# Kernel optimization log

Hardware: AMD Instinct MI355X
Metric: run time of the kernel (lower is better)

The kernel has to match this reference:

```python
import jax, jax.numpy as jnp
import numpy as np

N = 8192      # number of nodes; input feature dim == N (identity-style features)
HID = 200     # hidden dim hard-coded in GCNConv(adj.shape[0], 200)
OUT = 5       # out_dim (sentiment classes)


def setup_inputs() -> dict:
    key = jax.random.key(0)
    k1, k2, k3, k4 = jax.random.split(key, 4)
    x = jax.random.normal(k1, (N, N), dtype=jnp.float32)
    adj = jax.random.uniform(k2, (N, N), dtype=jnp.float32)
    W1 = jax.random.normal(k3, (N, HID), dtype=jnp.float32) * (1.0 / np.sqrt(N))
    b1 = jnp.zeros((HID,), dtype=jnp.float32)
    W2 = jax.random.normal(k4, (HID, OUT), dtype=jnp.float32) * (1.0 / np.sqrt(HID))
    b2 = jnp.zeros((OUT,), dtype=jnp.float32)
    return {"x": x, "adj": adj, "W1": W1, "b1": b1, "W2": W2, "b2": b2}


def gcn_conv(adj, x, W, b):
    # support = X @ W (cheap, small output dim), then propagate: adj @ support
    return adj @ (x @ W) + b


def reference(x, adj, W1, b1, W2, b2):
    h = jax.nn.relu(gcn_conv(adj, x, W1, b1))      # [N, 200]
    logits = gcn_conv(adj, h, W2, b2)              # [N, 5]
    return jax.nn.softmax(logits, axis=-1)
```

## Files before the change

kernel.cpp:

```cpp
#include <hip/hip_runtime.h>
#include <hip/hip_fp16.h>
#include <math.h>

#define NN   8192
#define KD   8192
#define HID  200
#define NP   224
#define OUTC 5

#define BM   128
#define BK   32
#define KS   8
#define KCH  (KD / KS)
#define NT   (KCH / BK)
#define TUB  896

typedef _Float16 f16;
typedef __attribute__((ext_vector_type(4))) _Float16 f16x4;
typedef __attribute__((ext_vector_type(8))) _Float16 f16x8;
typedef __attribute__((ext_vector_type(4))) float f32x4;

__device__ __forceinline__ int swzu(int r, int c) {
    return (r * 4 + (c ^ (r & 3))) ^ (r & 4);
}

__device__ __forceinline__ void fill16(const f16* g, f16* l) {
    __builtin_amdgcn_global_load_lds(
        (const __attribute__((address_space(1))) void*)g,
        (__attribute__((address_space(3))) void*)l, 16, 0, 0);
}

__global__ __launch_bounds__(256) void k_prep_w1(const float* __restrict__ W1,
                                                 f16* __restrict__ Bsw) {
    __shared__ float tile[64][65];
    const int bx = blockIdx.x;
    const int n0 = blockIdx.y * 64;
    const int k0 = bx * 64;
    const int t = threadIdx.x;
    #pragma unroll
    for (int q = 0; q < 4; ++q) {
        int idx4 = t + q * 256;
        int kk = idx4 >> 4, nn4 = (idx4 & 15) * 4;
        int n = n0 + nn4;
        float4 v = {0.f, 0.f, 0.f, 0.f};
        if (n + 4 <= HID) v = *(const float4*)(W1 + (size_t)(k0 + kk) * HID + n);
        tile[kk][nn4 + 0] = v.x; tile[kk][nn4 + 1] = v.y;
        tile[kk][nn4 + 2] = v.z; tile[kk][nn4 + 3] = v.w;
    }
    __syncthreads();
    #pragma unroll
    for (int p2 = 0; p2 < 2; ++p2) {
        int u = t + p2 * 256;
        int rl = u >> 3, cc = u & 7;
        int ktl = cc >> 2, c = cc & 3;
        int r = n0 + rl;
        if (r < NP) {
            f16x8 o;
            #pragma unroll
            for (int h = 0; h < 8; ++h) o[h] = (f16)tile[ktl * 32 + c * 8 + h][rl];
            *(f16x8*)(Bsw + ((size_t)(bx * 2 + ktl) * TUB + swzu(r, c)) * 8) = o;
        }
    }
}

__global__ __launch_bounds__(512, 4) void k_gemm(const float* __restrict__ A,
                                                 const f16* __restrict__ Bsw,
                                                 f16* __restrict__ CP) {
    __shared__ __align__(16) f16 Af0[BM * BK], Af1[BM * BK];
    __shared__ __align__(16) f16 Bf0[NP * BK], Bf1[NP * BK];

    const int t = threadIdx.x;
    const int lane = t & 63, wv = t >> 6;
    const int wm = wv >> 1, wn = wv & 1;
    const int l15 = lane & 15, g = lane >> 4;
    const int bid = blockIdx.x;
    const int ky = bid & 7;
    const int bx = bid >> 3;
    const int m0 = bx * BM;
    const int kt0 = ky * NT;
    const size_t kc0 = (size_t)ky * KCH;

    const int ar = t >> 2, aq = t & 3;
    const int au = swzu(ar, aq) * 8;
    const float* ap = A + (size_t)(m0 + ar) * KD + kc0 + (size_t)aq * 8;
    const f16* bsrc = Bsw + ((size_t)kt0 * TUB + (size_t)(wv * 64 + lane)) * 8;

    const int a0o = swzu(wm * 32 + l15, g) * 8;
    const int bo0 = swzu(wn * 112 + l15, g) * 8;

    f32x4 acc[2][7];
    #pragma unroll
    for (int m = 0; m < 2; ++m)
        #pragma unroll
        for (int n = 0; n < 7; ++n) acc[m][n] = (f32x4){0.f, 0.f, 0.f, 0.f};

    float4 va0, va1, vb0, vb1;
#define LOADA(i, V0, V1) { const float* p_ = ap + (size_t)(i) * BK;  \
        V0 = *(const float4*)p_; V1 = *(const float4*)(p_ + 4); }
#define CONV_STORE(AF, V0, V1) { f16x8 hh_;                                   \
        hh_[0]=(f16)V0.x; hh_[1]=(f16)V0.y; hh_[2]=(f16)V0.z; hh_[3]=(f16)V0.w; \
        hh_[4]=(f16)V1.x; hh_[5]=(f16)V1.y; hh_[6]=(f16)V1.z; hh_[7]=(f16)V1.w; \
        *(f16x8*)&AF[au] = hh_; }
#define FILLB(i, BF) { const f16* bs_ = bsrc + (size_t)(i) * (TUB * 8);  \
        fill16(bs_, &BF[(wv * 64) * 8]);                                 \
        if (wv < 6) fill16(bs_ + 512 * 8, &BF[(512 + wv * 64) * 8]); }
#define MFMA_PH(AF, BF) {                                                \
        f16x8 a0_ = *(const f16x8*)&AF[a0o];                             \
        f16x8 a1_ = *(const f16x8*)&AF[a0o + 512];                       \
        _Pragma("unroll")                                                \
        for (int n = 0; n < 7; ++n) {                                    \
            f16x8 b_ = *(const f16x8*)&BF[bo0 + n * 512];                \
            acc[0][n] = __builtin_amdgcn_mfma_f32_16x16x32_f16(a0_, b_, acc[0][n], 0, 0, 0); \
            acc[1][n] = __builtin_amdgcn_mfma_f32_16x16x32_f16(a1_, b_, acc[1][n], 0, 0, 0); } }

    LOADA(0, va0, va1); LOADA(1, vb0, vb1);
    FILLB(0, Bf0);
    CONV_STORE(Af0, va0, va1);
    asm volatile("s_waitcnt vmcnt(0) lgkmcnt(0)\n\ts_barrier" ::: "memory");

    #pragma unroll 1
    for (int ip = 0; ip < NT / 2 - 1; ++ip) {
        const int i = 2 * ip;
        FILLB(i + 1, Bf1);
        CONV_STORE(Af1, vb0, vb1);
        LOADA(i + 2, va0, va1);
        __builtin_amdgcn_s_setprio(1);
        MFMA_PH(Af0, Bf0);
        __builtin_amdgcn_s_setprio(0);
        asm volatile("s_waitcnt vmcnt(2) lgkmcnt(0)\n\ts_barrier" ::: "memory");
        FILLB(i + 2, Bf0);
        CONV_STORE(Af0, va0, va1);
        LOADA(i + 3, vb0, vb1);
        __builtin_amdgcn_s_setprio(1);
        MFMA_PH(Af1, Bf1);
        __builtin_amdgcn_s_setprio(0);
        asm volatile("s_waitcnt vmcnt(2) lgkmcnt(0)\n\ts_barrier" ::: "memory");
    }
    FILLB(NT - 1, Bf1);
    CONV_STORE(Af1, vb0, vb1);
    __builtin_amdgcn_s_setprio(1);
    MFMA_PH(Af0, Bf0);
    __builtin_amdgcn_s_setprio(0);
    asm volatile("s_waitcnt vmcnt(0) lgkmcnt(0)\n\ts_barrier" ::: "memory");
    MFMA_PH(Af1, Bf1);
#undef LOADA
#undef CONV_STORE
#undef FILLB
#undef MFMA_PH

    f16* o = CP + (size_t)ky * ((size_t)NN * NP);
    #pragma unroll
    for (int m = 0; m < 2; ++m) {
        #pragma unroll
        for (int n = 0; n < 7; ++n) {
            int rb = m0 + wm * 32 + m * 16 + g * 4;
            int c = wn * 112 + n * 16 + l15;
            #pragma unroll
            for (int r = 0; r < 4; ++r)
                o[(size_t)(rb + r) * NP + c] = (f16)acc[m][n][r];
        }
    }
}

__global__ __launch_bounds__(256) void k_combine_b(const f16* __restrict__ CP,
                                                   f16* __restrict__ Bsw) {
    __shared__ float tile[64][65];
    const size_t SZ = (size_t)NN * NP;
    const int bx = blockIdx.x;
    const int n0 = blockIdx.y * 64;
    const int k0 = bx * 64;
    const int t = threadIdx.x;
    #pragma unroll
    for (int q = 0; q < 4; ++q) {
        int idx4 = t + q * 256;
        int kk = idx4 >> 4, nn4 = (idx4 & 15) * 4;
        int n = n0 + nn4;
        float s0 = 0.f, s1 = 0.f, s2 = 0.f, s3 = 0.f;
        if (n < NP) {
            #pragma unroll
            for (int p = 0; p < KS; ++p) {
                f16x4 v = *(const f16x4*)(CP + (size_t)p * SZ + (size_t)(k0 + kk) * NP + n);
                s0 += (float)v[0]; s1 += (float)v[1]; s2 += (float)v[2]; s3 += (float)v[3];
            }
        }
        tile[kk][nn4 + 0] = s0; tile[kk][nn4 + 1] = s1;
        tile[kk][nn4 + 2] = s2; tile[kk][nn4 + 3] = s3;
    }
    __syncthreads();
    #pragma unroll
    for (int p2 = 0; p2 < 2; ++p2) {
        int u = t + p2 * 256;
        int rl = u >> 3, cc = u & 7;
        int ktl = cc >> 2, c = cc & 3;
        int r = n0 + rl;
        if (r < NP) {
            f16x8 o;
            #pragma unroll
            for (int h = 0; h < 8; ++h) o[h] = (f16)tile[ktl * 32 + c * 8 + h][rl];
            *(f16x8*)(Bsw + ((size_t)(bx * 2 + ktl) * TUB + swzu(r, c)) * 8) = o;
        }
    }
}

__global__ __launch_bounds__(256) void k_tail(const f16* __restrict__ CP,
                                              const float* __restrict__ b1,
                                              const float* __restrict__ W2,
                                              float* __restrict__ S2T) {
    const int tx = threadIdx.x;
    const int ty = threadIdx.y;
    const int row = blockIdx.x * 8 + ty;
    float s[OUTC] = {0.f, 0.f, 0.f, 0.f, 0.f};
    if (tx < 28) {
        const size_t SZ = (size_t)NN * NP;
        const size_t off = (size_t)row * NP + tx * 8;
        float h[8] = {0.f,0.f,0.f,0.f,0.f,0.f,0.f,0.f};
        #pragma unroll
        for (int p = 0; p < KS; ++p) {
            f16x8 v = *(const f16x8*)(CP + (size_t)p * SZ + off);
            #pragma unroll
            for (int j = 0; j < 8; ++j) h[j] += (float)v[j];
        }
        #pragma unroll
        for (int j = 0; j < 8; ++j) {
            int c = tx * 8 + j;
            if (c < HID) {
                float hv = fmaxf(h[j] + b1[c], 0.f);
                #pragma unroll
                for (int q = 0; q < OUTC; ++q) s[q] += hv * W2[c * OUTC + q];
            }
        }
    }
    #pragma unroll
    for (int q = 0; q < OUTC; ++q)
        #pragma unroll
        for (int off2 = 16; off2; off2 >>= 1) s[q] += __shfl_down(s[q], off2, 32);
    if (tx == 0) {
        #pragma unroll
        for (int q = 0; q < OUTC; ++q) S2T[(size_t)q * NN + row] = s[q];
    }
}

__global__ __launch_bounds__(256) void k_final(const float* __restrict__ adj,
                                               const float* __restrict__ S2T,
                                               const float* __restrict__ b2,
                                               float* __restrict__ out) {
    __shared__ float red[4][8][OUTC];
    const int t = threadIdx.x, wave = t >> 6, lane = t & 63;
    const int row0 = blockIdx.x * 8;
    float acc[8][OUTC];
    #pragma unroll
    for (int r = 0; r < 8; ++r)
        #pragma unroll
        for (int c = 0; c < OUTC; ++c) acc[r][c] = 0.f;

    for (int jj = 0; jj < 8; ++jj) {
        int kb = (t + jj * 256) * 4;
        float4 s2[OUTC];
        #pragma unroll
        for (int c = 0; c < OUTC; ++c) s2[c] = *(const float4*)(S2T + (size_t)c * NN + kb);
        #pragma unroll
        for (int r = 0; r < 8; ++r) {
            float4 a = *(const float4*)(adj + (size_t)(row0 + r) * KD + kb);
            #pragma unroll
            for (int c = 0; c < OUTC; ++c)
                acc[r][c] += a.x * s2[c].x + a.y * s2[c].y + a.z * s2[c].z + a.w * s2[c].w;
        }
    }
    #pragma unroll
    for (int r = 0; r < 8; ++r)
        #pragma unroll
        for (int c = 0; c < OUTC; ++c) {
            float v = acc[r][c];
            #pragma unroll
            for (int off = 32; off; off >>= 1) v += __shfl_down(v, off, 64);
            if (lane == 0) red[wave][r][c] = v;
        }
    __syncthreads();
    if (t < 8) {
        int r = t;
        float lg[OUTC];
        #pragma unroll
        for (int c = 0; c < OUTC; ++c)
            lg[c] = red[0][r][c] + red[1][r][c] + red[2][r][c] + red[3][r][c] + b2[c];
        float mx = lg[0];
        #pragma unroll
        for (int c = 1; c < OUTC; ++c) mx = fmaxf(mx, lg[c]);
        float e[OUTC], ssum = 0.f;
        #pragma unroll
        for (int c = 0; c < OUTC; ++c) { e[c] = expf(lg[c] - mx); ssum += e[c]; }
        float inv = 1.0f / ssum;
        #pragma unroll
        for (int c = 0; c < OUTC; ++c) out[(size_t)(row0 + r) * OUTC + c] = e[c] * inv;
    }
}

extern "C" void kernel_launch(void* const* d_in, const int* in_sizes, int n_in,
                              void* d_out, int out_size, void* d_ws, size_t ws_size,
                              hipStream_t stream) {
    const float* x   = (const float*)d_in[0];
    const float* adj = (const float*)d_in[1];
    const float* W1  = (const float*)d_in[2];
    const float* b1  = (const float*)d_in[3];
    const float* W2  = (const float*)d_in[4];
    const float* b2  = (const float*)d_in[5];
    float* out = (float*)d_out;

    char* ws = (char*)d_ws;
    const size_t BSZ = (size_t)NP * KD * sizeof(f16);
    f16*   BW1 = (f16*)(ws);
    f16*   BS1 = (f16*)(ws + BSZ);
    float* S2T = (float*)(ws + 2 * BSZ);
    f16*   CP  = (f16*)(ws + 2 * BSZ + 256 * 1024);

    k_prep_w1<<<dim3(128, 4), 256, 0, stream>>>(W1, BW1);
    k_gemm<<<dim3(512), 512, 0, stream>>>(x, BW1, CP);
    k_combine_b<<<dim3(128, 4), 256, 0, stream>>>(CP, BS1);
    k_gemm<<<dim3(512), 512, 0, stream>>>(adj, BS1, CP);
    k_tail<<<dim3(NN / 8), dim3(32, 8), 0, stream>>>(CP, b1, W2, S2T);
    k_final<<<dim3(NN / 8), 256, 0, stream>>>(adj, S2T, b2, out);
}
```

Baseline: 252.6 us.

## Feed A fragments straight from global into registers, halve GEMM tile rows

The split-K GEMM no longer stages the fp32 A tile through LDS. Each lane loads its own A rows from global memory, converts them to fp16 in registers and feeds them straight to the MFMAs, so only B is double-buffered in LDS. To make this work the block tile drops to 64 rows with 256 threads (grid doubled), and the B staging tile is padded to 1024 units so four clean async fills cover it. Cross-wave A sharing through LDS is gone, so A loads are less coalesced and each A element is read by both column waves. The loop tail now re-fetches the last tile redundantly rather than using a separate epilogue.

```diff
diff --git a/kernel.cpp b/kernel.cpp
--- a/kernel.cpp
+++ b/kernel.cpp
@@ -8,12 +8,12 @@
 #define NP   224
 #define OUTC 5
 
-#define BM   128
+#define BM   64
 #define BK   32
 #define KS   8
 #define KCH  (KD / KS)
 #define NT   (KCH / BK)
-#define TUB  896
+#define TUB  1024
 
 typedef _Float16 f16;
 typedef __attribute__((ext_vector_type(4))) _Float16 f16x4;
@@ -63,11 +63,10 @@
     }
 }
 
-__global__ __launch_bounds__(512, 4) void k_gemm(const float* __restrict__ A,
+__global__ __launch_bounds__(256, 4) void k_gemm(const float* __restrict__ A,
                                                  const f16* __restrict__ Bsw,
                                                  f16* __restrict__ CP) {
-    __shared__ __align__(16) f16 Af0[BM * BK], Af1[BM * BK];
-    __shared__ __align__(16) f16 Bf0[NP * BK], Bf1[NP * BK];
+    __shared__ __align__(16) f16 Bf0[TUB * 8], Bf1[TUB * 8];
 
     const int t = threadIdx.x;
     const int lane = t & 63, wv = t >> 6;
@@ -80,13 +79,13 @@
     const int kt0 = ky * NT;
     const size_t kc0 = (size_t)ky * KCH;
 
-    const int ar = t >> 2, aq = t & 3;
-    const int au = swzu(ar, aq) * 8;
-    const float* ap = A + (size_t)(m0 + ar) * KD + kc0 + (size_t)aq * 8;
-    const f16* bsrc = Bsw + ((size_t)kt0 * TUB + (size_t)(wv * 64 + lane)) * 8;
-
-    const int a0o = swzu(wm * 32 + l15, g) * 8;
-    const int bo0 = swzu(wn * 112 + l15, g) * 8;
+    const float* ap0 = A + (size_t)(m0 + wm * 32 + l15) * KD + kc0 + (size_t)g * 8;
+    const float* ap1 = ap0 + (size_t)16 * KD;
+    const f16* bsrc = Bsw + ((size_t)kt0 * TUB + (size_t)t) * 8;
+
+    int bofs[7];
+    #pragma unroll
+    for (int n = 0; n < 7; ++n) bofs[n] = swzu(wn * 112 + n * 16 + l15, g) * 8;
 
     f32x4 acc[2][7];
     #pragma unroll
@@ -94,58 +93,63 @@
         #pragma unroll
         for (int n = 0; n < 7; ++n) acc[m][n] = (f32x4){0.f, 0.f, 0.f, 0.f};
 
-    float4 va0, va1, vb0, vb1;
-#define LOADA(i, V0, V1) { const float* p_ = ap + (size_t)(i) * BK;  \
-        V0 = *(const float4*)p_; V1 = *(const float4*)(p_ + 4); }
-#define CONV_STORE(AF, V0, V1) { f16x8 hh_;                                   \
-        hh_[0]=(f16)V0.x; hh_[1]=(f16)V0.y; hh_[2]=(f16)V0.z; hh_[3]=(f16)V0.w; \
-        hh_[4]=(f16)V1.x; hh_[5]=(f16)V1.y; hh_[6]=(f16)V1.z; hh_[7]=(f16)V1.w; \
-        *(f16x8*)&AF[au] = hh_; }
+    float4 va0, va1, va2, va3, vb0, vb1, vb2, vb3;
+#define LOADA(i, V0, V1, V2, V3) { size_t o_ = (size_t)(i) * BK;            \
+        V0 = *(const float4*)(ap0 + o_); V1 = *(const float4*)(ap0 + o_ + 4); \
+        V2 = *(const float4*)(ap1 + o_); V3 = *(const float4*)(ap1 + o_ + 4); }
 #define FILLB(i, BF) { const f16* bs_ = bsrc + (size_t)(i) * (TUB * 8);  \
-        fill16(bs_, &BF[(wv * 64) * 8]);                                 \
-        if (wv < 6) fill16(bs_ + 512 * 8, &BF[(512 + wv * 64) * 8]); }
-#define MFMA_PH(AF, BF) {                                                \
-        f16x8 a0_ = *(const f16x8*)&AF[a0o];                             \
-        f16x8 a1_ = *(const f16x8*)&AF[a0o + 512];                       \
-        _Pragma("unroll")                                                \
-        for (int n = 0; n < 7; ++n) {                                    \
-            f16x8 b_ = *(const f16x8*)&BF[bo0 + n * 512];                \
-            acc[0][n] = __builtin_amdgcn_mfma_f32_16x16x32_f16(a0_, b_, acc[0][n], 0, 0, 0); \
-            acc[1][n] = __builtin_amdgcn_mfma_f32_16x16x32_f16(a1_, b_, acc[1][n], 0, 0, 0); } }
-
-    LOADA(0, va0, va1); LOADA(1, vb0, vb1);
+        fill16(bs_,            &BF[(t      ) * 8]);                      \
+        fill16(bs_ + 256 * 8,  &BF[(t + 256) * 8]);                      \
+        fill16(bs_ + 512 * 8,  &BF[(t + 512) * 8]);                      \
+        fill16(bs_ + 768 * 8,  &BF[(t + 768) * 8]); }
+#define CVT(F0, F1, V0, V1, V2, V3) {                                       \
+        F0[0]=(f16)V0.x; F0[1]=(f16)V0.y; F0[2]=(f16)V0.z; F0[3]=(f16)V0.w;  \
+        F0[4]=(f16)V1.x; F0[5]=(f16)V1.y; F0[6]=(f16)V1.z; F0[7]=(f16)V1.w;  \
+        F1[0]=(f16)V2.x; F1[1]=(f16)V2.y; F1[2]=(f16)V2.z; F1[3]=(f16)V2.w;  \
+        F1[4]=(f16)V3.x; F1[5]=(f16)V3.y; F1[6]=(f16)V3.z; F1[7]=(f16)V3.w; }
+#define MFMA_PH(BF, F0, F1) {                                               \
+        _Pragma("unroll")                                                   \
+        for (int n = 0; n < 7; ++n) {                                       \
+            f16x8 b_ = *(const f16x8*)&BF[bofs[n]];                         \
+            acc[0][n] = __builtin_amdgcn_mfma_f32_16x16x32_f16(F0, b_, acc[0][n], 0, 0, 0); \
+            acc[1][n] = __builtin_amdgcn_mfma_f32_16x16x32_f16(F1, b_, acc[1][n], 0, 0, 0); } }
+
     FILLB(0, Bf0);
-    CONV_STORE(Af0, va0, va1);
-    asm volatile("s_waitcnt vmcnt(0) lgkmcnt(0)\n\ts_barrier" ::: "memory");
-
-    #pragma unroll 1
-    for (int ip = 0; ip < NT / 2 - 1; ++ip) {
+    __builtin_amdgcn_sched_barrier(0);
+    LOADA(0, va0, va1, va2, va3);
+    LOADA(1, vb0, vb1, vb2, vb3);
+    __builtin_amdgcn_sched_barrier(0);
+    asm volatile("s_waitcnt vmcnt(8)\n\ts_barrier" ::: "memory");
+
+    for (int ip = 0; ip < NT / 2; ++ip) {
         const int i = 2 * ip;
+        const int iL2 = (i + 2 < NT) ? i + 2 : NT - 1;
+        const int iF2 = iL2;
+        const int iL3 = (i + 3 < NT) ? i + 3 : NT - 1;
+        f16x8 fa0, fa1;
+        CVT(fa0, fa1, va0, va1, va2, va3);
         FILLB(i + 1, Bf1);
-        CONV_STORE(Af1, vb0, vb1);
-        LOADA(i + 2, va0, va1);
+        __builtin_amdgcn_sched_barrier(0);
+        LOADA(iL2, va0, va1, va2, va3);
+        __builtin_amdgcn_sched_barrier(0);
         __builtin_amdgcn_s_setprio(1);
-        MFMA_PH(Af0, Bf0);
+        MFMA_PH(Bf0, fa0, fa1);
         __builtin_amdgcn_s_setprio(0);
-        asm volatile("s_waitcnt vmcnt(2) lgkmcnt(0)\n\ts_barrier" ::: "memory");
-        FILLB(i + 2, Bf0);
-        CONV_STORE(Af0, va0, va1);
-        LOADA(i + 3, vb0, vb1);
+        asm volatile("s_waitcnt vmcnt(4) lgkmcnt(0)\n\ts_barrier" ::: "memory");
+        f16x8 fb0, fb1;
+        CVT(fb0, fb1, vb0, vb1, vb2, vb3);
+        FILLB(iF2, Bf0);
+        __builtin_amdgcn_sched_barrier(0);
+        LOADA(iL3, vb0, vb1, vb2, vb3);
+        __builtin_amdgcn_sched_barrier(0);
         __builtin_amdgcn_s_setprio(1);
-        MFMA_PH(Af1, Bf1);
+        MFMA_PH(Bf1, fb0, fb1);
         __builtin_amdgcn_s_setprio(0);
-        asm volatile("s_waitcnt vmcnt(2) lgkmcnt(0)\n\ts_barrier" ::: "memory");
-    }
-    FILLB(NT - 1, Bf1);
-    CONV_STORE(Af1, vb0, vb1);
-    __builtin_amdgcn_s_setprio(1);
-    MFMA_PH(Af0, Bf0);
-    __builtin_amdgcn_s_setprio(0);
-    asm volatile("s_waitcnt vmcnt(0) lgkmcnt(0)\n\ts_barrier" ::: "memory");
-    MFMA_PH(Af1, Bf1);
+        asm volatile("s_waitcnt vmcnt(4) lgkmcnt(0)\n\ts_barrier" ::: "memory");
+    }
 #undef LOADA
-#undef CONV_STORE
 #undef FILLB
+#undef CVT
 #undef MFMA_PH
 
     f16* o = CP + (size_t)ky * ((size_t)NN * NP);
@@ -306,16 +310,16 @@
     float* out = (float*)d_out;
 
     char* ws = (char*)d_ws;
-    const size_t BSZ = (size_t)NP * KD * sizeof(f16);
+    const size_t BSZ = (size_t)256 * TUB * 16;
     f16*   BW1 = (f16*)(ws);
     f16*   BS1 = (f16*)(ws + BSZ);
     float* S2T = (float*)(ws + 2 * BSZ);
     f16*   CP  = (f16*)(ws + 2 * BSZ + 256 * 1024);
 
     k_prep_w1<<<dim3(128, 4), 256, 0, stream>>>(W1, BW1);
-    k_gemm<<<dim3(512), 512, 0, stream>>>(x, BW1, CP);
+    k_gemm<<<dim3(1024), 256, 0, stream>>>(x, BW1, CP);
     k_combine_b<<<dim3(128, 4), 256, 0, stream>>>(CP, BS1);
-    k_gemm<<<dim3(512), 512, 0, stream>>>(adj, BS1, CP);
+    k_gemm<<<dim3(1024), 256, 0, stream>>>(adj, BS1, CP);
     k_tail<<<dim3(NN / 8), dim3(32, 8), 0, stream>>>(CP, b1, W2, S2T);
     k_final<<<dim3(NN / 8), 256, 0, stream>>>(adj, S2T, b2, out);
 }
```

New measurement: 422.1 us. 1.67x slower.
